# Optimization experiments

Measured on AMD Instinct MI355X. Metric: run time of the kernel, lower is better.

The kernel has to match this reference:

```python
import jax, jax.numpy as jnp
import numpy as np

DIM = 512; VOCAB = 10000; DEPTH = 3
DSTATE = 16; DCONV = 4; EXPAND = 2; HEADS = 8
DINNER = EXPAND * DIM            # 1024
DTRANK = (DIM + 15) // 16        # 32 (mamba_ssm: ceil(d_model/16))
B = 4; L = 1024; CTX = 98
EPS = 1e-5


def layer_norm(x, g, b):
    mu = jnp.mean(x, -1, keepdims=True)
    var = jnp.var(x, -1, keepdims=True)
    return (x - mu) / jnp.sqrt(var + EPS) * g + b


def silu(x):
    return x * jax.nn.sigmoid(x)


def mamba_block(x, in_w, conv_w, conv_b, xproj_w, dt_w, dt_b, A_log, D_skip, out_w):
    # x: [B,L,DIM]
    Bb = x.shape[0]
    xz = x @ in_w.T                              # [B,L,2*DINNER]
    u, z = jnp.split(xz, 2, -1)                  # each [B,L,DINNER]
    # causal depthwise conv1d (pad left d_conv-1)
    uc = jnp.transpose(u, (0, 2, 1))             # [B,DINNER,L]
    uc = jax.lax.conv_general_dilated(
        uc, conv_w, (1,), [(DCONV - 1, 0)],
        dimension_numbers=('NCH', 'OIH', 'NCH'),
        feature_group_count=DINNER)
    u = silu(jnp.transpose(uc, (0, 2, 1)) + conv_b)   # [B,L,DINNER]
    x_dbl = u @ xproj_w.T                        # [B,L,DTRANK+2*DSTATE]
    dt, Bm, Cm = jnp.split(x_dbl, [DTRANK, DTRANK + DSTATE], -1)
    delta = jax.nn.softplus(dt @ dt_w.T + dt_b)  # [B,L,DINNER]
    A = -jnp.exp(A_log)                          # [DINNER,DSTATE]

    def step(h, inp):
        d_t, B_t, C_t, u_t = inp                 # [B,DINNER],[B,DSTATE],[B,DSTATE],[B,DINNER]
        dA = jnp.exp(d_t[..., None] * A)         # [B,DINNER,DSTATE]
        h = dA * h + (d_t * u_t)[..., None] * B_t[:, None, :]
        y_t = jnp.einsum('bds,bs->bd', h, C_t)
        return h, y_t

    h0 = jnp.zeros((Bb, DINNER, DSTATE), x.dtype)
    xs = (jnp.swapaxes(delta, 0, 1), jnp.swapaxes(Bm, 0, 1),
          jnp.swapaxes(Cm, 0, 1), jnp.swapaxes(u, 0, 1))
    _, ys = jax.lax.scan(step, h0, xs)           # ys: [L,B,DINNER]
    y = jnp.swapaxes(ys, 0, 1) + u * D_skip
    y = y * silu(z)
    return y @ out_w.T                           # [B,L,DIM]


def cross_attention(q_in, ctx, in_w, in_b, out_w, out_b):
    Bb, Ln, _ = q_in.shape
    S = ctx.shape[1]
    dh = DIM // HEADS
    wq, wk, wv = jnp.split(in_w, 3, 0)
    bq, bk, bv = jnp.split(in_b, 3, 0)
    q = (q_in @ wq.T + bq).reshape(Bb, Ln, HEADS, dh)
    k = (ctx @ wk.T + bk).reshape(Bb, S, HEADS, dh)
    v = (ctx @ wv.T + bv).reshape(Bb, S, HEADS, dh)
    scale = 1.0 / np.sqrt(dh).astype(np.float32)
    scores = jnp.einsum('blhd,bshd->bhls', q, k) * scale
    attn = jax.nn.softmax(scores, axis=-1)       # [B,H,L,S]
    out = jnp.einsum('bhls,bshd->blhd', attn, v).reshape(Bb, Ln, DIM)
    out = out @ out_w.T + out_b
    return out, attn.mean(axis=1)                # torch MHA averages heads


def setup_inputs() -> dict:
    key = jax.random.key(0)
    ks = jax.random.split(key, 16)
    s = 0.02
    d = {}
    d['x'] = jax.random.randint(ks[0], (B, L), 0, VOCAB)
    d['context'] = jax.random.normal(ks[1], (B, CTX, DIM), jnp.float32)
    d['tok_emb'] = jax.random.normal(ks[2], (VOCAB, DIM), jnp.float32) * s
    d['pos_emb'] = jax.random.normal(ks[3], (1, 1024, DIM), jnp.float32) * s
    d['ln1_g'] = jnp.ones((DEPTH, DIM)); d['ln1_b'] = jnp.zeros((DEPTH, DIM))
    d['in_w'] = jax.random.normal(ks[4], (DEPTH, 2 * DINNER, DIM), jnp.float32) * s
    d['conv_w'] = jax.random.normal(ks[5], (DEPTH, DINNER, 1, DCONV), jnp.float32) * 0.1
    d['conv_b'] = jnp.zeros((DEPTH, DINNER))
    d['xproj_w'] = jax.random.normal(ks[6], (DEPTH, DTRANK + 2 * DSTATE, DINNER), jnp.float32) * s
    d['dt_w'] = jax.random.normal(ks[7], (DEPTH, DINNER, DTRANK), jnp.float32) * 0.1
    d['dt_b'] = jax.random.normal(ks[8], (DEPTH, DINNER), jnp.float32) * 0.1
    # S4D-real init: A_log = log(1..d_state)
    A_log = jnp.log(jnp.arange(1, DSTATE + 1, dtype=jnp.float32))
    d['A_log'] = jnp.broadcast_to(A_log, (DEPTH, DINNER, DSTATE)).copy()
    d['D_skip'] = jnp.ones((DEPTH, DINNER))
    d['mamba_out_w'] = jax.random.normal(ks[9], (DEPTH, DIM, DINNER), jnp.float32) * s
    d['ln2_g'] = jnp.ones((DEPTH, DIM)); d['ln2_b'] = jnp.zeros((DEPTH, DIM))
    d['attn_in_w'] = jax.random.normal(ks[10], (DEPTH, 3 * DIM, DIM), jnp.float32) * s
    d['attn_in_b'] = jnp.zeros((DEPTH, 3 * DIM))
    d['attn_out_w'] = jax.random.normal(ks[11], (DEPTH, DIM, DIM), jnp.float32) * s
    d['attn_out_b'] = jnp.zeros((DEPTH, DIM))
    d['lnf_g'] = jnp.ones((DIM,)); d['lnf_b'] = jnp.zeros((DIM,))
    d['logit_w'] = jax.random.normal(ks[12], (VOCAB, DIM), jnp.float32) * s
    d['logit_b'] = jnp.zeros((VOCAB,))
    return d


def reference(x, context, tok_emb, pos_emb, ln1_g, ln1_b, in_w, conv_w, conv_b,
              xproj_w, dt_w, dt_b, A_log, D_skip, mamba_out_w, ln2_g, ln2_b,
              attn_in_w, attn_in_b, attn_out_w, attn_out_b, lnf_g, lnf_b,
              logit_w, logit_b):
    n = x.shape[1]
    h = tok_emb[x] + pos_emb[:, :n]              # [B,L,DIM]
    all_attn = []
    for i in range(DEPTH):
        h_norm = layer_norm(h, ln1_g[i], ln1_b[i])
        h = h + mamba_block(h_norm, in_w[i], conv_w[i], conv_b[i], xproj_w[i],
                            dt_w[i], dt_b[i], A_log[i], D_skip[i], mamba_out_w[i])
        h_norm = layer_norm(h, ln2_g[i], ln2_b[i])
        attn_out, attn_w = cross_attention(h_norm, context, attn_in_w[i],
                                           attn_in_b[i], attn_out_w[i], attn_out_b[i])
        all_attn.append(attn_w)
        h = h + attn_out
    h = layer_norm(h, lnf_g, lnf_b)
    logits = h @ logit_w.T + logit_b             # [B,L,VOCAB]
    return (logits, tuple(all_attn))
```

## Files before the change

kernel.cpp:

```cpp
#include <hip/hip_runtime.h>
#include <hip/hip_bf16.h>
#include <math.h>

#define DIM 512
#define VOCAB 10000
#define NPAD 10240
#define DEPTH 3
#define DSTATE 16
#define DCONV 4
#define DINNER 1024
#define DTRANK 32
#define BATCH 4
#define SEQ 1024
#define CTX 98
#define HEADS 8
#define DH 64
#define NTOK (BATCH*SEQ)
#define NC 32
#define LC 32
#define KVLD 1024
#define CTXPAD 512

typedef __attribute__((ext_vector_type(8))) short short8;
typedef __attribute__((ext_vector_type(4))) float f32x4;

__device__ __forceinline__ float sigmoidf_(float x){ return 1.f/(1.f+__expf(-x)); }

__device__ __forceinline__ void gload_lds16(const void* g, void* s){
    __builtin_amdgcn_global_load_lds(
        (const __attribute__((address_space(1))) void*)g,
        (__attribute__((address_space(3))) void*)s, 16, 0, 0);
}

__global__ __launch_bounds__(256)
void f2bf_kernel(const float* __restrict__ in, __hip_bfloat16* __restrict__ out)
{
    int i = (blockIdx.x*256 + threadIdx.x)*8;
    float4 a = *(const float4*)(in+i);
    float4 b = *(const float4*)(in+i+4);
    union { __hip_bfloat16 v[8]; short8 s; } o;
    o.v[0]=__float2bfloat16(a.x); o.v[1]=__float2bfloat16(a.y);
    o.v[2]=__float2bfloat16(a.z); o.v[3]=__float2bfloat16(a.w);
    o.v[4]=__float2bfloat16(b.x); o.v[5]=__float2bfloat16(b.y);
    o.v[6]=__float2bfloat16(b.z); o.v[7]=__float2bfloat16(b.w);
    *(short8*)(out+i) = o.s;
}

__global__ __launch_bounds__(128)
void embed_kernel(const int* __restrict__ x,
                  const float* __restrict__ tok_emb,
                  const float* __restrict__ pos_emb,
                  float* __restrict__ h)
{
    int row = blockIdx.x;
    int l = row & (SEQ-1);
    int tok = x[row];
    const float4* te = (const float4*)(tok_emb + (size_t)tok*DIM);
    const float4* pe = (const float4*)(pos_emb + (size_t)l*DIM);
    float4* hp = (float4*)(h + (size_t)row*DIM);
    int i = threadIdx.x;
    float4 a = te[i], b = pe[i];
    hp[i] = make_float4(a.x+b.x, a.y+b.y, a.z+b.z, a.w+b.w);
}

__global__ __launch_bounds__(256)
void layernorm_kernel(const float* __restrict__ in, const float* __restrict__ g,
                      const float* __restrict__ b, __hip_bfloat16* __restrict__ out)
{
    int row = blockIdx.x;
    const float* xr = in + (size_t)row*DIM;
    int t = threadIdx.x;
    float2 v = *(const float2*)(xr + t*2);
    float s  = v.x + v.y;
    float s2 = v.x*v.x + v.y*v.y;
    #pragma unroll
    for (int o=32;o>=1;o>>=1){ s += __shfl_xor(s,o); s2 += __shfl_xor(s2,o); }
    __shared__ float ss[4], ss2[4];
    int w = t>>6;
    if ((t&63)==0){ ss[w]=s; ss2[w]=s2; }
    __syncthreads();
    s  = ss[0]+ss[1]+ss[2]+ss[3];
    s2 = ss2[0]+ss2[1]+ss2[2]+ss2[3];
    float mu  = s * (1.f/DIM);
    float var = s2 * (1.f/DIM) - mu*mu;
    float rstd = rsqrtf(var + 1e-5f);
    float2 gg = *(const float2*)(g + t*2);
    float2 bb = *(const float2*)(b + t*2);
    __hip_bfloat162 o2;
    o2.x = __float2bfloat16((v.x-mu)*rstd*gg.x + bb.x);
    o2.y = __float2bfloat16((v.y-mu)*rstd*gg.y + bb.y);
    *(__hip_bfloat162*)(out + (size_t)row*DIM + t*2) = o2;
}

template<int BIAS, int RES, int NCHECK, int OUTBF>
__global__ __launch_bounds__(256)
void gemm_bf16(const __hip_bfloat16* __restrict__ A, int lda,
               const __hip_bfloat16* __restrict__ W, int ldw,
               const float* __restrict__ bias,
               void* __restrict__ Cv, int ldc, int Nstore, int K)
{
    __shared__ __hip_bfloat16 As[128*32];
    __shared__ __hip_bfloat16 Ws[128*32];
    int t = threadIdx.x;
    int w = t >> 6, l = t & 63;
    int m0 = blockIdx.y*128, n0 = blockIdx.x*128;
    int wm = (w>>1)*64, wn = (w&1)*64;
    int lrow = l & 15, lq = l >> 4;
    f32x4 acc[4][4];
    #pragma unroll
    for (int i=0;i<4;i++)
        #pragma unroll
        for (int j=0;j<4;j++)
            acc[i][j] = (f32x4){0.f,0.f,0.f,0.f};

    for (int k0 = 0; k0 < K; k0 += 32){
        __syncthreads();
        #pragma unroll
        for (int it = 0; it < 2; ++it){
            int p = it*256 + t;
            int r = p >> 2, c = (p & 3)*8;
            gload_lds16(A + (size_t)(m0+r)*lda + k0 + c, As + p*8);
            gload_lds16(W + (size_t)(n0+r)*ldw + k0 + c, Ws + p*8);
        }
        __syncthreads();
        short8 a[4], b[4];
        #pragma unroll
        for (int mt=0;mt<4;mt++)
            a[mt] = *(const short8*)(As + (wm + mt*16 + lrow)*32 + lq*8);
        #pragma unroll
        for (int nt=0;nt<4;nt++)
            b[nt] = *(const short8*)(Ws + (wn + nt*16 + lrow)*32 + lq*8);
        #pragma unroll
        for (int mt=0;mt<4;mt++)
            #pragma unroll
            for (int nt=0;nt<4;nt++)
                acc[mt][nt] = __builtin_amdgcn_mfma_f32_16x16x32_bf16(
                    a[mt], b[nt], acc[mt][nt], 0, 0, 0);
    }
    #pragma unroll
    for (int nt=0;nt<4;nt++){
        int col = n0 + wn + nt*16 + lrow;
        if (NCHECK && col >= Nstore) continue;
        float bv = BIAS ? bias[col] : 0.f;
        #pragma unroll
        for (int mt=0;mt<4;mt++){
            #pragma unroll
            for (int r=0;r<4;r++){
                int row = m0 + wm + mt*16 + lq*4 + r;
                float v = acc[mt][nt][r] + bv;
                if (OUTBF){
                    __hip_bfloat16* cp = (__hip_bfloat16*)Cv + (size_t)row*ldc + col;
                    *cp = __float2bfloat16(v);
                } else {
                    float* cp = (float*)Cv + (size_t)row*ldc + col;
                    if (RES) v += *cp;
                    *cp = v;
                }
            }
        }
    }
}

template<int ACT, int BIAS, int RES>
__global__ __launch_bounds__(256)
void gemm_f32(const float* __restrict__ A, int lda,
              const float* __restrict__ W, int ldw,
              const float* __restrict__ bias,
              float* __restrict__ C, int ldc,
              int M, int N, int K)
{
    __shared__ float As[16][64];
    __shared__ float Ws[16][64];
    int t = threadIdx.x;
    int tx = t & 15, ty = t >> 4;
    int m0 = blockIdx.y * 64, n0 = blockIdx.x * 64;
    int loadRow = t >> 2;
    int loadK   = (t & 3) << 2;
    float acc[4][4] = {};
    for (int k0 = 0; k0 < K; k0 += 16) {
        {
            int gr = m0 + loadRow;
            float4 a4 = make_float4(0.f,0.f,0.f,0.f);
            if (gr < M) a4 = *(const float4*)(A + (size_t)gr*lda + k0 + loadK);
            As[loadK+0][loadRow] = a4.x;
            As[loadK+1][loadRow] = a4.y;
            As[loadK+2][loadRow] = a4.z;
            As[loadK+3][loadRow] = a4.w;
            int gn = n0 + loadRow;
            float4 w4 = make_float4(0.f,0.f,0.f,0.f);
            if (gn < N) w4 = *(const float4*)(W + (size_t)gn*ldw + k0 + loadK);
            Ws[loadK+0][loadRow] = w4.x;
            Ws[loadK+1][loadRow] = w4.y;
            Ws[loadK+2][loadRow] = w4.z;
            Ws[loadK+3][loadRow] = w4.w;
        }
        __syncthreads();
        #pragma unroll
        for (int k = 0; k < 16; ++k) {
            float4 a4 = *(const float4*)&As[k][ty<<2];
            float4 w4 = *(const float4*)&Ws[k][tx<<2];
            float a[4] = {a4.x,a4.y,a4.z,a4.w};
            float w[4] = {w4.x,w4.y,w4.z,w4.w};
            #pragma unroll
            for (int i=0;i<4;i++)
                #pragma unroll
                for (int j=0;j<4;j++)
                    acc[i][j] = fmaf(a[i], w[j], acc[i][j]);
        }
        __syncthreads();
    }
    #pragma unroll
    for (int i=0;i<4;i++){
        int row = m0 + (ty<<2) + i;
        if (row >= M) continue;
        #pragma unroll
        for (int j=0;j<4;j++){
            int col = n0 + (tx<<2) + j;
            if (col >= N) continue;
            float v = acc[i][j];
            if (BIAS) v += bias[col];
            if (ACT==1) v = (v > 20.f) ? v : log1pf(__expf(v));
            float* cp = C + (size_t)row*ldc + col;
            if (RES) v += *cp;
            *cp = v;
        }
    }
}

__global__ __launch_bounds__(256)
void conv_silu_kernel(const float* __restrict__ xz, const float* __restrict__ cw,
                      const float* __restrict__ cb, float* __restrict__ u,
                      __hip_bfloat16* __restrict__ ubf)
{
    int idx = blockIdx.x*256 + threadIdx.x;
    int d = idx & (DINNER-1);
    int row = idx >> 10;
    int l = row & (SEQ-1);
    int bbase = row - l;
    float acc = cb[d];
    #pragma unroll
    for (int k=0;k<DCONV;k++){
        int ls = l - (DCONV-1) + k;
        if (ls >= 0)
            acc = fmaf(xz[((size_t)(bbase+ls))*(2*DINNER) + d], cw[d*DCONV+k], acc);
    }
    float uv = acc * sigmoidf_(acc);
    u[idx] = uv;
    ubf[idx] = __float2bfloat16(uv);
}

__global__ __launch_bounds__(256)
void scan_pass1(const float* __restrict__ delta, const float* __restrict__ u,
                const float* __restrict__ xdbl, const float* __restrict__ A_log,
                float* __restrict__ hend, float* __restrict__ dsum_out)
{
    __shared__ float bc[LC][32];
    int c = blockIdx.x;
    int b = blockIdx.y >> 2, dg = blockIdx.y & 3;
    int t = threadIdx.x;
    int d = dg*256 + t;
    int rowbase = b*SEQ + c*LC;
    for (int idx = t; idx < LC*32; idx += 256){
        int r = idx >> 5, j = idx & 31;
        bc[r][j] = xdbl[(size_t)(rowbase + r)*64 + DTRANK + j];
    }
    float Av[DSTATE];
    #pragma unroll
    for (int s4 = 0; s4 < 4; ++s4){
        float4 a4 = *(const float4*)(A_log + (size_t)d*DSTATE + s4*4);
        Av[s4*4+0] = -__expf(a4.x);
        Av[s4*4+1] = -__expf(a4.y);
        Av[s4*4+2] = -__expf(a4.z);
        Av[s4*4+3] = -__expf(a4.w);
    }
    __syncthreads();
    float h[DSTATE] = {};
    float ds = 0.f;
    for (int tt = 0; tt < LC; ++tt){
        size_t row = (size_t)(rowbase + tt);
        float dlt = delta[row*DINNER + d];
        float uv  = u[row*DINNER + d];
        ds += dlt;
        float du = dlt*uv;
        #pragma unroll
        for (int s = 0; s < DSTATE; ++s)
            h[s] = fmaf(__expf(dlt*Av[s]), h[s], du*bc[tt][s]);
    }
    size_t base = ((size_t)(b*NC + c)*DINNER + d)*DSTATE;
    #pragma unroll
    for (int s4=0;s4<4;s4++)
        *(float4*)(hend + base + s4*4) =
            make_float4(h[s4*4],h[s4*4+1],h[s4*4+2],h[s4*4+3]);
    dsum_out[(size_t)(b*NC+c)*DINNER + d] = ds;
}

__global__ __launch_bounds__(256)
void scan_pass2(const float* __restrict__ hend, const float* __restrict__ dsum,
                const float* __restrict__ A_log, float* __restrict__ hin)
{
    int gid = blockIdx.x*256 + threadIdx.x;
    int s = gid & 15;
    int bd = gid >> 4;
    int d = bd & (DINNER-1);
    int b = bd >> 10;
    float Av = -__expf(A_log[(size_t)d*DSTATE + s]);
    float h = 0.f;
    for (int c = 0; c < NC; ++c){
        size_t idx = ((size_t)(b*NC + c)*DINNER + d)*DSTATE + s;
        hin[idx] = h;
        h = fmaf(__expf(Av*dsum[(size_t)(b*NC+c)*DINNER + d]), h, hend[idx]);
    }
}

__global__ __launch_bounds__(256)
void scan_pass3(const float* __restrict__ delta, const float* __restrict__ u,
                const float* __restrict__ xdbl, const float* __restrict__ xz,
                const float* __restrict__ A_log, const float* __restrict__ D_skip,
                const float* __restrict__ hin, __hip_bfloat16* __restrict__ y)
{
    __shared__ float bc[LC][32];
    int c = blockIdx.x;
    int b = blockIdx.y >> 2, dg = blockIdx.y & 3;
    int t = threadIdx.x;
    int d = dg*256 + t;
    int rowbase = b*SEQ + c*LC;
    for (int idx = t; idx < LC*32; idx += 256){
        int r = idx >> 5, j = idx & 31;
        bc[r][j] = xdbl[(size_t)(rowbase + r)*64 + DTRANK + j];
    }
    float Av[DSTATE];
    #pragma unroll
    for (int s4 = 0; s4 < 4; ++s4){
        float4 a4 = *(const float4*)(A_log + (size_t)d*DSTATE + s4*4);
        Av[s4*4+0] = -__expf(a4.x);
        Av[s4*4+1] = -__expf(a4.y);
        Av[s4*4+2] = -__expf(a4.z);
        Av[s4*4+3] = -__expf(a4.w);
    }
    float h[DSTATE];
    size_t hbase = ((size_t)(b*NC + c)*DINNER + d)*DSTATE;
    #pragma unroll
    for (int s4=0;s4<4;s4++){
        float4 h4 = *(const float4*)(hin + hbase + s4*4);
        h[s4*4+0]=h4.x; h[s4*4+1]=h4.y; h[s4*4+2]=h4.z; h[s4*4+3]=h4.w;
    }
    float Dv = D_skip[d];
    __syncthreads();
    for (int tt = 0; tt < LC; ++tt){
        size_t row = (size_t)(rowbase + tt);
        float dlt = delta[row*DINNER + d];
        float uv  = u[row*DINNER + d];
        float du = dlt*uv;
        float yv = 0.f;
        #pragma unroll
        for (int s = 0; s < DSTATE; ++s){
            h[s] = fmaf(__expf(dlt*Av[s]), h[s], du*bc[tt][s]);
            yv = fmaf(h[s], bc[tt][16+s], yv);
        }
        float zv = xz[row*(2*DINNER) + DINNER + d];
        y[row*DINNER + d] = __float2bfloat16((yv + uv*Dv) * (zv * sigmoidf_(zv)));
    }
}

#define QS_OFF 0
#define KS_OFF 16384
#define VT_OFF 30720
#define PT_OFF 47104
#define SMEM_BYTES 79872

__device__ __forceinline__ int swz(int row, int byteoff){
    return byteoff ^ ((row & 7) << 4);
}

__global__ __launch_bounds__(512)
void attn_mfma_kernel(const __hip_bfloat16* __restrict__ q,
                      const __hip_bfloat16* __restrict__ kv,
                      __hip_bfloat16* __restrict__ outp,
                      float* __restrict__ Pg)
{
    __shared__ alignas(16) char smem[SMEM_BYTES];
    int t = threadIdx.x;
    int bh = blockIdx.x;
    int b = bh >> 3, h = bh & 7;
    int lrow0 = blockIdx.y * 128;
    size_t grow0 = (size_t)b*SEQ + lrow0;

    #pragma unroll
    for (int it = 0; it < 6; ++it)
        *(f32x4*)(smem + VT_OFF + (it*512 + t)*16) = (f32x4){0.f,0.f,0.f,0.f};
    __syncthreads();

    const __hip_bfloat16* qb = q + grow0*DIM + h*DH;
    #pragma unroll
    for (int it = 0; it < 2; ++it){
        int cidx = it*512 + t;
        int row = cidx >> 3, c8 = cidx & 7;
        short8 a = *(const short8*)(qb + (size_t)row*DIM + c8*8);
        *(short8*)(smem + QS_OFF + row*128 + swz(row, c8*16)) = a;
    }
    const __hip_bfloat16* kb = kv + (size_t)(b*CTX)*KVLD + h*DH;
    #pragma unroll
    for (int it = 0; it < 2; ++it){
        int cidx = it*512 + t;
        if (cidx < 112*8){
            int row = cidx >> 3, c8 = cidx & 7;
            short8 a = (short8){0,0,0,0,0,0,0,0};
            if (row < CTX) a = *(const short8*)(kb + (size_t)row*KVLD + c8*8);
            *(short8*)(smem + KS_OFF + row*128 + swz(row, c8*16)) = a;
        }
    }
    const __hip_bfloat16* vb = kv + (size_t)(b*CTX)*KVLD + DIM + h*DH;
    #pragma unroll
    for (int it = 0; it < 4; ++it){
        int c = it*512 + t;
        if (c < 1600){
            int d = c & 63, s4 = c >> 6;
            union { unsigned short hh[4]; unsigned long long u; } pk;
            #pragma unroll
            for (int j = 0; j < 4; ++j){
                int s = s4*4 + j;
                pk.hh[j] = (s < CTX) ? *(const unsigned short*)(vb + (size_t)s*KVLD + d) : 0;
            }
            *(unsigned long long*)(smem + VT_OFF + d*256 + swz(d, s4*8)) = pk.u;
        }
    }
    __syncthreads();

    int w = t >> 6, l = t & 63;
    int lr = l & 15, lq = l >> 4;
    f32x4 acc[7];
    #pragma unroll
    for (int nt = 0; nt < 7; ++nt) acc[nt] = (f32x4){0.f,0.f,0.f,0.f};
    #pragma unroll
    for (int kk = 0; kk < 2; ++kk){
        int arow = w*16 + lr;
        short8 af = *(const short8*)(smem + QS_OFF + arow*128 + swz(arow, kk*64 + lq*16));
        #pragma unroll
        for (int nt = 0; nt < 7; ++nt){
            int brow = nt*16 + lr;
            short8 bf = *(const short8*)(smem + KS_OFF + brow*128 + swz(brow, kk*64 + lq*16));
            acc[nt] = __builtin_amdgcn_mfma_f32_16x16x32_bf16(af, bf, acc[nt], 0, 0, 0);
        }
    }

    float* Pgp = Pg + ((size_t)bh*SEQ + lrow0)*CTX;
    #pragma unroll
    for (int r = 0; r < 4; ++r){
        int row = w*16 + lq*4 + r;
        float vals[7];
        #pragma unroll
        for (int nt = 0; nt < 7; ++nt) vals[nt] = acc[nt][r] * 0.125f;
        if (lr >= 2) vals[6] = -1e30f;
        float m = vals[0];
        #pragma unroll
        for (int nt = 1; nt < 7; ++nt) m = fmaxf(m, vals[nt]);
        #pragma unroll
        for (int o = 8; o >= 1; o >>= 1) m = fmaxf(m, __shfl_xor(m, o));
        float ssum = 0.f;
        #pragma unroll
        for (int nt = 0; nt < 7; ++nt){ vals[nt] = __expf(vals[nt] - m); ssum += vals[nt]; }
        #pragma unroll
        for (int o = 8; o >= 1; o >>= 1) ssum += __shfl_xor(ssum, o);
        float inv = 1.f / ssum;
        #pragma unroll
        for (int nt = 0; nt < 7; ++nt){
            float p = vals[nt] * inv;
            int col = nt*16 + lr;
            *(__hip_bfloat16*)(smem + PT_OFF + row*256 + swz(row, col*2)) = __float2bfloat16(p);
            if (col < CTX) Pgp[(size_t)row*CTX + col] = p;
        }
    }
    __syncthreads();

    f32x4 acc2[4];
    #pragma unroll
    for (int nt = 0; nt < 4; ++nt) acc2[nt] = (f32x4){0.f,0.f,0.f,0.f};
    #pragma unroll
    for (int kk = 0; kk < 4; ++kk){
        int arow = w*16 + lr;
        short8 af = *(const short8*)(smem + PT_OFF + arow*256 + swz(arow, kk*64 + lq*16));
        #pragma unroll
        for (int nt = 0; nt < 4; ++nt){
            int brow = nt*16 + lr;
            short8 bf = *(const short8*)(smem + VT_OFF + brow*256 + swz(brow, kk*64 + lq*16));
            acc2[nt] = __builtin_amdgcn_mfma_f32_16x16x32_bf16(af, bf, acc2[nt], 0, 0, 0);
        }
    }
    #pragma unroll
    for (int nt = 0; nt < 4; ++nt){
        int col = h*DH + nt*16 + lr;
        #pragma unroll
        for (int r = 0; r < 4; ++r){
            int row = w*16 + lq*4 + r;
            outp[(grow0 + row)*DIM + col] = __float2bfloat16(acc2[nt][r]);
        }
    }
}

__global__ __launch_bounds__(256)
void attn_mean_kernel(const float* __restrict__ Pg, float* __restrict__ am)
{
    int idx = blockIdx.x*256 + threadIdx.x;
    int row = idx / CTX;
    int s = idx - row*CTX;
    int b = row >> 10;
    int l = row & (SEQ-1);
    const float* p = Pg + ((size_t)(b*HEADS)*SEQ + l)*CTX + s;
    float acc = 0.f;
    #pragma unroll
    for (int h = 0; h < HEADS; ++h) acc += p[(size_t)h*SEQ*CTX];
    am[idx] = acc * 0.125f;
}

extern "C" void kernel_launch(void* const* d_in, const int* in_sizes, int n_in,
                              void* d_out, int out_size, void* d_ws, size_t ws_size,
                              hipStream_t stream)
{
    (void)in_sizes; (void)n_in; (void)out_size; (void)ws_size;
    const int*   x        = (const int*)  d_in[0];
    const float* context  = (const float*)d_in[1];
    const float* tok_emb  = (const float*)d_in[2];
    const float* pos_emb  = (const float*)d_in[3];
    const float* ln1_g    = (const float*)d_in[4];
    const float* ln1_b    = (const float*)d_in[5];
    const float* in_w     = (const float*)d_in[6];
    const float* conv_w   = (const float*)d_in[7];
    const float* conv_b   = (const float*)d_in[8];
    const float* xproj_w  = (const float*)d_in[9];
    const float* dt_w     = (const float*)d_in[10];
    const float* dt_b     = (const float*)d_in[11];
    const float* A_log    = (const float*)d_in[12];
    const float* D_skip   = (const float*)d_in[13];
    const float* out_w    = (const float*)d_in[14];
    const float* ln2_g    = (const float*)d_in[15];
    const float* ln2_b    = (const float*)d_in[16];
    const float* ain_w    = (const float*)d_in[17];
    const float* ain_b    = (const float*)d_in[18];
    const float* aout_w   = (const float*)d_in[19];
    const float* aout_b   = (const float*)d_in[20];
    const float* lnf_g    = (const float*)d_in[21];
    const float* lnf_b    = (const float*)d_in[22];
    const float* logit_w  = (const float*)d_in[23];
    const float* logit_b  = (const float*)d_in[24];
    float* out = (float*)d_out;

    float* ws = (float*)d_ws;
    size_t off = 0;
    float* hbuf  = ws + off;  off += (size_t)NTOK*DIM;
    float* ubuf  = ws + off;  off += (size_t)NTOK*DINNER;
    float* xdbl  = ws + off;  off += (size_t)NTOK*64;
    float* dbuf  = ws + off;  off += (size_t)NTOK*DINNER;
    __hip_bfloat16* tnorm_bf   = (__hip_bfloat16*)(ws + off); off += (size_t)NTOK*DIM/2;
    __hip_bfloat16* logit_w_bf = (__hip_bfloat16*)(ws + off); off += (size_t)NPAD*DIM/2;
    float* Pgbuf = dbuf;

    float* ob = out;
    float* xz    = ob;                 ob += (size_t)NTOK*2*DINNER;
    float* hend  = ob;                 ob += (size_t)BATCH*NC*DINNER*DSTATE;
    float* hinb  = ob;                 ob += (size_t)BATCH*NC*DINNER*DSTATE;
    float* dsumb = ob;                 ob += (size_t)BATCH*NC*DINNER;
    __hip_bfloat16* bfp = (__hip_bfloat16*)ob;
    __hip_bfloat16* in_w_bf   = bfp;   bfp += (size_t)DEPTH*2*DINNER*DIM;
    __hip_bfloat16* out_w_bf  = bfp;   bfp += (size_t)DEPTH*DIM*DINNER;
    __hip_bfloat16* ainw_bf   = bfp;   bfp += (size_t)DEPTH*3*DIM*DIM;
    __hip_bfloat16* aoutw_bf  = bfp;   bfp += (size_t)DEPTH*DIM*DIM;
    __hip_bfloat16* ybuf_bf   = bfp;   bfp += (size_t)NTOK*DINNER;
    __hip_bfloat16* abuf_bf   = bfp;   bfp += (size_t)NTOK*DIM;
    __hip_bfloat16* qbf       = bfp;   bfp += (size_t)NTOK*DIM;
    __hip_bfloat16* ubf       = bfp;   bfp += (size_t)NTOK*DINNER;
    __hip_bfloat16* ctx_bf    = bfp;   bfp += (size_t)CTXPAD*DIM;
    __hip_bfloat16* kv_bf     = bfp;   bfp += (size_t)CTXPAD*KVLD;
    __hip_bfloat16* xprojw_bf = bfp;   bfp += (size_t)DEPTH*128*DINNER;

    f2bf_kernel<<<(DEPTH*2*DINNER*DIM)/2048, 256, 0, stream>>>(in_w, in_w_bf);
    f2bf_kernel<<<(DEPTH*DIM*DINNER)/2048, 256, 0, stream>>>(out_w, out_w_bf);
    f2bf_kernel<<<(DEPTH*3*DIM*DIM)/2048, 256, 0, stream>>>(ain_w, ainw_bf);
    f2bf_kernel<<<(DEPTH*DIM*DIM)/2048, 256, 0, stream>>>(aout_w, aoutw_bf);
    f2bf_kernel<<<(VOCAB*DIM)/2048, 256, 0, stream>>>(logit_w, logit_w_bf);
    hipMemsetAsync(logit_w_bf + (size_t)VOCAB*DIM, 0,
                   (size_t)(NPAD-VOCAB)*DIM*sizeof(__hip_bfloat16), stream);
    f2bf_kernel<<<(BATCH*CTX*DIM)/2048, 256, 0, stream>>>(context, ctx_bf);
    hipMemsetAsync(ctx_bf + (size_t)BATCH*CTX*DIM, 0,
                   (size_t)(CTXPAD - BATCH*CTX)*DIM*sizeof(__hip_bfloat16), stream);
    hipMemsetAsync(xprojw_bf, 0, (size_t)DEPTH*128*DINNER*sizeof(__hip_bfloat16), stream);
    for (int i = 0; i < DEPTH; ++i)
        f2bf_kernel<<<(64*DINNER)/2048, 256, 0, stream>>>(
            xproj_w + (size_t)i*64*DINNER, xprojw_bf + (size_t)i*128*DINNER);

    embed_kernel<<<NTOK, 128, 0, stream>>>(x, tok_emb, pos_emb, hbuf);

    float* attn_out_base = out + (size_t)NTOK*VOCAB;

    for (int i = 0; i < DEPTH; ++i){
        const float* Ai = A_log + (size_t)i*DINNER*DSTATE;
        layernorm_kernel<<<NTOK, 256, 0, stream>>>(hbuf, ln1_g + i*DIM, ln1_b + i*DIM, tnorm_bf);
        gemm_bf16<0,0,0,0><<<dim3(2*DINNER/128, NTOK/128), 256, 0, stream>>>(
            tnorm_bf, DIM, in_w_bf + (size_t)i*2*DINNER*DIM, DIM, nullptr,
            xz, 2*DINNER, 2*DINNER, DIM);
        conv_silu_kernel<<<(NTOK*DINNER)/256, 256, 0, stream>>>(
            xz, conv_w + (size_t)i*DINNER*DCONV, conv_b + i*DINNER, ubuf, ubf);
        gemm_bf16<0,0,1,0><<<dim3(1, NTOK/128), 256, 0, stream>>>(
            ubf, DINNER, xprojw_bf + (size_t)i*128*DINNER, DINNER, nullptr,
            xdbl, 64, 64, DINNER);
        gemm_f32<1,1,0><<<dim3(DINNER/64, NTOK/64), 256, 0, stream>>>(
            xdbl, 64, dt_w + (size_t)i*DINNER*DTRANK, DTRANK, dt_b + i*DINNER,
            dbuf, DINNER, NTOK, DINNER, DTRANK);
        scan_pass1<<<dim3(NC, BATCH*4), 256, 0, stream>>>(
            dbuf, ubuf, xdbl, Ai, hend, dsumb);
        scan_pass2<<<(BATCH*DINNER*DSTATE)/256, 256, 0, stream>>>(
            hend, dsumb, Ai, hinb);
        scan_pass3<<<dim3(NC, BATCH*4), 256, 0, stream>>>(
            dbuf, ubuf, xdbl, xz, Ai, D_skip + i*DINNER, hinb, ybuf_bf);
        gemm_bf16<0,1,0,0><<<dim3(DIM/128, NTOK/128), 256, 0, stream>>>(
            ybuf_bf, DINNER, out_w_bf + (size_t)i*DIM*DINNER, DINNER, nullptr,
            hbuf, DIM, DIM, DINNER);
        layernorm_kernel<<<NTOK, 256, 0, stream>>>(hbuf, ln2_g + i*DIM, ln2_b + i*DIM, tnorm_bf);
        gemm_bf16<1,0,0,1><<<dim3(DIM/128, NTOK/128), 256, 0, stream>>>(
            tnorm_bf, DIM, ainw_bf + (size_t)i*3*DIM*DIM, DIM, ain_b + (size_t)i*3*DIM,
            qbf, DIM, DIM, DIM);
        gemm_bf16<1,0,0,1><<<dim3(KVLD/128, CTXPAD/128), 256, 0, stream>>>(
            ctx_bf, DIM, ainw_bf + (size_t)i*3*DIM*DIM + (size_t)DIM*DIM, DIM,
            ain_b + (size_t)i*3*DIM + DIM, kv_bf, KVLD, KVLD, DIM);
        attn_mfma_kernel<<<dim3(BATCH*HEADS, SEQ/128), 512, 0, stream>>>(
            qbf, kv_bf, abuf_bf, Pgbuf);
        attn_mean_kernel<<<(NTOK*CTX)/256, 256, 0, stream>>>(
            Pgbuf, attn_out_base + (size_t)i*NTOK*CTX);
        gemm_bf16<1,1,0,0><<<dim3(DIM/128, NTOK/128), 256, 0, stream>>>(
            abuf_bf, DIM, aoutw_bf + (size_t)i*DIM*DIM, DIM, aout_b + i*DIM,
            hbuf, DIM, DIM, DIM);
    }
    layernorm_kernel<<<NTOK, 256, 0, stream>>>(hbuf, lnf_g, lnf_b, tnorm_bf);
    gemm_bf16<1,0,1,0><<<dim3(NPAD/128, NTOK/128), 256, 0, stream>>>(
        tnorm_bf, DIM, logit_w_bf, DIM, logit_b, out, VOCAB, VOCAB, DIM);
}
```

Baseline: 1.131 ms.

## Merge weight conversions, batch KV projections across layers, split-K the x_proj GEMM

All fp32-to-bf16 weight and context conversions and the zero-padding memsets are merged into one prep kernel. The three per-layer K/V projections of the fixed context become a single batched GEMM launch, using a new z-dimension offset scheme in gemm_bf16. The narrow x_proj GEMM, which previously ran only 32 blocks, is split four ways along K into partial buffers and summed by a small reduce kernel. This is meant to cut launch count and raise parallelism, at the cost of extra partial-sum traffic and a larger kv buffer.

```diff
diff --git a/kernel.cpp b/kernel.cpp
--- a/kernel.cpp
+++ b/kernel.cpp
@@ -20,6 +20,7 @@
 #define LC 32
 #define KVLD 1024
 #define CTXPAD 512
+#define XKS 4
 
 typedef __attribute__((ext_vector_type(8))) short short8;
 typedef __attribute__((ext_vector_type(4))) float f32x4;
@@ -32,18 +33,66 @@
         (__attribute__((address_space(3))) void*)s, 16, 0, 0);
 }
 
-__global__ __launch_bounds__(256)
-void f2bf_kernel(const float* __restrict__ in, __hip_bfloat16* __restrict__ out)
-{
-    int i = (blockIdx.x*256 + threadIdx.x)*8;
-    float4 a = *(const float4*)(in+i);
-    float4 b = *(const float4*)(in+i+4);
-    union { __hip_bfloat16 v[8]; short8 s; } o;
+__device__ __forceinline__ void cvt8(const float* __restrict__ s, __hip_bfloat16* __restrict__ d){
+    float4 a = *(const float4*)s;
+    float4 b = *(const float4*)(s+4);
+    union { __hip_bfloat16 v[8]; short8 x; } o;
     o.v[0]=__float2bfloat16(a.x); o.v[1]=__float2bfloat16(a.y);
     o.v[2]=__float2bfloat16(a.z); o.v[3]=__float2bfloat16(a.w);
     o.v[4]=__float2bfloat16(b.x); o.v[5]=__float2bfloat16(b.y);
     o.v[6]=__float2bfloat16(b.z); o.v[7]=__float2bfloat16(b.w);
-    *(short8*)(out+i) = o.s;
+    *(short8*)d = o.x;
+}
+__device__ __forceinline__ void zero8(__hip_bfloat16* __restrict__ d){
+    *(short8*)d = (short8){0,0,0,0,0,0,0,0};
+}
+
+#define N_INW   (DEPTH*2*DINNER*DIM)
+#define N_OUTW  (DEPTH*DIM*DINNER)
+#define N_AINW  (DEPTH*3*DIM*DIM)
+#define N_AOUTW (DEPTH*DIM*DIM)
+#define N_LOGIT (NPAD*DIM)
+#define N_CTX   (CTXPAD*DIM)
+#define N_XPROJ (DEPTH*128*DINNER)
+#define N_PREP_TOTAL (N_INW+N_OUTW+N_AINW+N_AOUTW+N_LOGIT+N_CTX+N_XPROJ)
+
+__global__ __launch_bounds__(256)
+void prep_kernel(const float* __restrict__ in_w,   __hip_bfloat16* __restrict__ in_w_bf,
+                 const float* __restrict__ out_w,  __hip_bfloat16* __restrict__ out_w_bf,
+                 const float* __restrict__ ain_w,  __hip_bfloat16* __restrict__ ainw_bf,
+                 const float* __restrict__ aout_w, __hip_bfloat16* __restrict__ aoutw_bf,
+                 const float* __restrict__ logit_w,__hip_bfloat16* __restrict__ logit_w_bf,
+                 const float* __restrict__ context,__hip_bfloat16* __restrict__ ctx_bf,
+                 const float* __restrict__ xproj_w,__hip_bfloat16* __restrict__ xprojw_bf)
+{
+    int i = (blockIdx.x*256 + threadIdx.x)*8;
+    if (i < N_INW){ cvt8(in_w + i, in_w_bf + i); return; }
+    i -= N_INW;
+    if (i < N_OUTW){ cvt8(out_w + i, out_w_bf + i); return; }
+    i -= N_OUTW;
+    if (i < N_AINW){ cvt8(ain_w + i, ainw_bf + i); return; }
+    i -= N_AINW;
+    if (i < N_AOUTW){ cvt8(aout_w + i, aoutw_bf + i); return; }
+    i -= N_AOUTW;
+    if (i < N_LOGIT){
+        if (i < VOCAB*DIM) cvt8(logit_w + i, logit_w_bf + i);
+        else zero8(logit_w_bf + i);
+        return;
+    }
+    i -= N_LOGIT;
+    if (i < N_CTX){
+        if (i < BATCH*CTX*DIM) cvt8(context + i, ctx_bf + i);
+        else zero8(ctx_bf + i);
+        return;
+    }
+    i -= N_CTX;
+    {
+        int layer = i >> 17;
+        int rem   = i & 131071;
+        int inrow = rem >> 10;
+        if (inrow < 64) cvt8(xproj_w + (layer<<16) + rem, xprojw_bf + i);
+        else            zero8(xprojw_bf + i);
+    }
 }
 
 __global__ __launch_bounds__(128)
@@ -97,11 +146,16 @@
 void gemm_bf16(const __hip_bfloat16* __restrict__ A, int lda,
                const __hip_bfloat16* __restrict__ W, int ldw,
                const float* __restrict__ bias,
-               void* __restrict__ Cv, int ldc, int Nstore, int K)
+               void* __restrict__ Cv, int ldc, int Nstore, int K,
+               size_t az, size_t wz, size_t cz, size_t bz)
 {
     __shared__ __hip_bfloat16 As[128*32];
     __shared__ __hip_bfloat16 Ws[128*32];
     int t = threadIdx.x;
+    int z = blockIdx.z;
+    const __hip_bfloat16* Ap = A + (size_t)z*az;
+    const __hip_bfloat16* Wp = W + (size_t)z*wz;
+    size_t coff = (size_t)z*cz;
     int w = t >> 6, l = t & 63;
     int m0 = blockIdx.y*128, n0 = blockIdx.x*128;
     int wm = (w>>1)*64, wn = (w&1)*64;
@@ -119,8 +173,8 @@
         for (int it = 0; it < 2; ++it){
             int p = it*256 + t;
             int r = p >> 2, c = (p & 3)*8;
-            gload_lds16(A + (size_t)(m0+r)*lda + k0 + c, As + p*8);
-            gload_lds16(W + (size_t)(n0+r)*ldw + k0 + c, Ws + p*8);
+            gload_lds16(Ap + (size_t)(m0+r)*lda + k0 + c, As + p*8);
+            gload_lds16(Wp + (size_t)(n0+r)*ldw + k0 + c, Ws + p*8);
         }
         __syncthreads();
         short8 a[4], b[4];
@@ -141,7 +195,7 @@
     for (int nt=0;nt<4;nt++){
         int col = n0 + wn + nt*16 + lrow;
         if (NCHECK && col >= Nstore) continue;
-        float bv = BIAS ? bias[col] : 0.f;
+        float bv = BIAS ? bias[(size_t)z*bz + col] : 0.f;
         #pragma unroll
         for (int mt=0;mt<4;mt++){
             #pragma unroll
@@ -149,16 +203,29 @@
                 int row = m0 + wm + mt*16 + lq*4 + r;
                 float v = acc[mt][nt][r] + bv;
                 if (OUTBF){
-                    __hip_bfloat16* cp = (__hip_bfloat16*)Cv + (size_t)row*ldc + col;
+                    __hip_bfloat16* cp = (__hip_bfloat16*)Cv + coff + (size_t)row*ldc + col;
                     *cp = __float2bfloat16(v);
                 } else {
-                    float* cp = (float*)Cv + (size_t)row*ldc + col;
+                    float* cp = (float*)Cv + coff + (size_t)row*ldc + col;
                     if (RES) v += *cp;
                     *cp = v;
                 }
             }
         }
     }
+}
+
+__global__ __launch_bounds__(256)
+void xreduce_kernel(const float* __restrict__ p, float* __restrict__ o)
+{
+    int i = (blockIdx.x*256 + threadIdx.x)*4;
+    const size_t S = (size_t)NTOK*64;
+    float4 a = *(const float4*)(p+i);
+    float4 b = *(const float4*)(p+i+S);
+    float4 c = *(const float4*)(p+i+2*S);
+    float4 d = *(const float4*)(p+i+3*S);
+    *(float4*)(o+i) = make_float4(a.x+b.x+c.x+d.x, a.y+b.y+c.y+d.y,
+                                  a.z+b.z+c.z+d.z, a.w+b.w+c.w+d.w);
 }
 
 template<int ACT, int BIAS, int RES>
@@ -550,6 +617,7 @@
     float* ubuf  = ws + off;  off += (size_t)NTOK*DINNER;
     float* xdbl  = ws + off;  off += (size_t)NTOK*64;
     float* dbuf  = ws + off;  off += (size_t)NTOK*DINNER;
+    float* xpart = ws + off;  off += (size_t)XKS*NTOK*64;
     __hip_bfloat16* tnorm_bf   = (__hip_bfloat16*)(ws + off); off += (size_t)NTOK*DIM/2;
     __hip_bfloat16* logit_w_bf = (__hip_bfloat16*)(ws + off); off += (size_t)NPAD*DIM/2;
     float* Pgbuf = dbuf;
@@ -560,34 +628,28 @@
     float* hinb  = ob;                 ob += (size_t)BATCH*NC*DINNER*DSTATE;
     float* dsumb = ob;                 ob += (size_t)BATCH*NC*DINNER;
     __hip_bfloat16* bfp = (__hip_bfloat16*)ob;
-    __hip_bfloat16* in_w_bf   = bfp;   bfp += (size_t)DEPTH*2*DINNER*DIM;
-    __hip_bfloat16* out_w_bf  = bfp;   bfp += (size_t)DEPTH*DIM*DINNER;
-    __hip_bfloat16* ainw_bf   = bfp;   bfp += (size_t)DEPTH*3*DIM*DIM;
-    __hip_bfloat16* aoutw_bf  = bfp;   bfp += (size_t)DEPTH*DIM*DIM;
+    __hip_bfloat16* in_w_bf   = bfp;   bfp += (size_t)N_INW;
+    __hip_bfloat16* out_w_bf  = bfp;   bfp += (size_t)N_OUTW;
+    __hip_bfloat16* ainw_bf   = bfp;   bfp += (size_t)N_AINW;
+    __hip_bfloat16* aoutw_bf  = bfp;   bfp += (size_t)N_AOUTW;
     __hip_bfloat16* ybuf_bf   = bfp;   bfp += (size_t)NTOK*DINNER;
     __hip_bfloat16* abuf_bf   = bfp;   bfp += (size_t)NTOK*DIM;
     __hip_bfloat16* qbf       = bfp;   bfp += (size_t)NTOK*DIM;
     __hip_bfloat16* ubf       = bfp;   bfp += (size_t)NTOK*DINNER;
-    __hip_bfloat16* ctx_bf    = bfp;   bfp += (size_t)CTXPAD*DIM;
-    __hip_bfloat16* kv_bf     = bfp;   bfp += (size_t)CTXPAD*KVLD;
-    __hip_bfloat16* xprojw_bf = bfp;   bfp += (size_t)DEPTH*128*DINNER;
-
-    f2bf_kernel<<<(DEPTH*2*DINNER*DIM)/2048, 256, 0, stream>>>(in_w, in_w_bf);
-    f2bf_kernel<<<(DEPTH*DIM*DINNER)/2048, 256, 0, stream>>>(out_w, out_w_bf);
-    f2bf_kernel<<<(DEPTH*3*DIM*DIM)/2048, 256, 0, stream>>>(ain_w, ainw_bf);
-    f2bf_kernel<<<(DEPTH*DIM*DIM)/2048, 256, 0, stream>>>(aout_w, aoutw_bf);
-    f2bf_kernel<<<(VOCAB*DIM)/2048, 256, 0, stream>>>(logit_w, logit_w_bf);
-    hipMemsetAsync(logit_w_bf + (size_t)VOCAB*DIM, 0,
-                   (size_t)(NPAD-VOCAB)*DIM*sizeof(__hip_bfloat16), stream);
-    f2bf_kernel<<<(BATCH*CTX*DIM)/2048, 256, 0, stream>>>(context, ctx_bf);
-    hipMemsetAsync(ctx_bf + (size_t)BATCH*CTX*DIM, 0,
-                   (size_t)(CTXPAD - BATCH*CTX)*DIM*sizeof(__hip_bfloat16), stream);
-    hipMemsetAsync(xprojw_bf, 0, (size_t)DEPTH*128*DINNER*sizeof(__hip_bfloat16), stream);
-    for (int i = 0; i < DEPTH; ++i)
-        f2bf_kernel<<<(64*DINNER)/2048, 256, 0, stream>>>(
-            xproj_w + (size_t)i*64*DINNER, xprojw_bf + (size_t)i*128*DINNER);
+    __hip_bfloat16* ctx_bf    = bfp;   bfp += (size_t)N_CTX;
+    __hip_bfloat16* kv_bf     = bfp;   bfp += (size_t)DEPTH*CTXPAD*KVLD;
+    __hip_bfloat16* xprojw_bf = bfp;   bfp += (size_t)N_XPROJ;
+
+    prep_kernel<<<N_PREP_TOTAL/2048, 256, 0, stream>>>(
+        in_w, in_w_bf, out_w, out_w_bf, ain_w, ainw_bf, aout_w, aoutw_bf,
+        logit_w, logit_w_bf, context, ctx_bf, xproj_w, xprojw_bf);
 
     embed_kernel<<<NTOK, 128, 0, stream>>>(x, tok_emb, pos_emb, hbuf);
+
+    gemm_bf16<1,0,0,1><<<dim3(KVLD/128, CTXPAD/128, DEPTH), 256, 0, stream>>>(
+        ctx_bf, DIM, ainw_bf + (size_t)DIM*DIM, DIM, ain_b + DIM,
+        kv_bf, KVLD, KVLD, DIM,
+        0, (size_t)3*DIM*DIM, (size_t)CTXPAD*KVLD, (size_t)3*DIM);
 
     float* attn_out_base = out + (size_t)NTOK*VOCAB;
 
@@ -596,12 +658,14 @@
         layernorm_kernel<<<NTOK, 256, 0, stream>>>(hbuf, ln1_g + i*DIM, ln1_b + i*DIM, tnorm_bf);
         gemm_bf16<0,0,0,0><<<dim3(2*DINNER/128, NTOK/128), 256, 0, stream>>>(
             tnorm_bf, DIM, in_w_bf + (size_t)i*2*DINNER*DIM, DIM, nullptr,
-            xz, 2*DINNER, 2*DINNER, DIM);
+            xz, 2*DINNER, 2*DINNER, DIM, 0, 0, 0, 0);
         conv_silu_kernel<<<(NTOK*DINNER)/256, 256, 0, stream>>>(
             xz, conv_w + (size_t)i*DINNER*DCONV, conv_b + i*DINNER, ubuf, ubf);
-        gemm_bf16<0,0,1,0><<<dim3(1, NTOK/128), 256, 0, stream>>>(
+        gemm_bf16<0,0,1,0><<<dim3(1, NTOK/128, XKS), 256, 0, stream>>>(
             ubf, DINNER, xprojw_bf + (size_t)i*128*DINNER, DINNER, nullptr,
-            xdbl, 64, 64, DINNER);
+            xpart, 64, 64, DINNER/XKS,
+            (size_t)(DINNER/XKS), (size_t)(DINNER/XKS), (size_t)NTOK*64, 0);
+        xreduce_kernel<<<(NTOK*64)/1024, 256, 0, stream>>>(xpart, xdbl);
         gemm_f32<1,1,0><<<dim3(DINNER/64, NTOK/64), 256, 0, stream>>>(
             xdbl, 64, dt_w + (size_t)i*DINNER*DTRANK, DTRANK, dt_b + i*DINNER,
             dbuf, DINNER, NTOK, DINNER, DTRANK);
@@ -613,23 +677,20 @@
             dbuf, ubuf, xdbl, xz, Ai, D_skip + i*DINNER, hinb, ybuf_bf);
         gemm_bf16<0,1,0,0><<<dim3(DIM/128, NTOK/128), 256, 0, stream>>>(
             ybuf_bf, DINNER, out_w_bf + (size_t)i*DIM*DINNER, DINNER, nullptr,
-            hbuf, DIM, DIM, DINNER);
+            hbuf, DIM, DIM, DINNER, 0, 0, 0, 0);
         layernorm_kernel<<<NTOK, 256, 0, stream>>>(hbuf, ln2_g + i*DIM, ln2_b + i*DIM, tnorm_bf);
         gemm_bf16<1,0,0,1><<<dim3(DIM/128, NTOK/128), 256, 0, stream>>>(
             tnorm_bf, DIM, ainw_bf + (size_t)i*3*DIM*DIM, DIM, ain_b + (size_t)i*3*DIM,
-            qbf, DIM, DIM, DIM);
-        gemm_bf16<1,0,0,1><<<dim3(KVLD/128, CTXPAD/128), 256, 0, stream>>>(
-            ctx_bf, DIM, ainw_bf + (size_t)i*3*DIM*DIM + (size_t)DIM*DIM, DIM,
-            ain_b + (size_t)i*3*DIM + DIM, kv_bf, KVLD, KVLD, DIM);
+            qbf, DIM, DIM, DIM, 0, 0, 0, 0);
         attn_mfma_kernel<<<dim3(BATCH*HEADS, SEQ/128), 512, 0, stream>>>(
-            qbf, kv_bf, abuf_bf, Pgbuf);
+            qbf, kv_bf + (size_t)i*CTXPAD*KVLD, abuf_bf, Pgbuf);
         attn_mean_kernel<<<(NTOK*CTX)/256, 256, 0, stream>>>(
             Pgbuf, attn_out_base + (size_t)i*NTOK*CTX);
         gemm_bf16<1,1,0,0><<<dim3(DIM/128, NTOK/128), 256, 0, stream>>>(
             abuf_bf, DIM, aoutw_bf + (size_t)i*DIM*DIM, DIM, aout_b + i*DIM,
-            hbuf, DIM, DIM, DIM);
+            hbuf, DIM, DIM, DIM, 0, 0, 0, 0);
     }
     layernorm_kernel<<<NTOK, 256, 0, stream>>>(hbuf, lnf_g, lnf_b, tnorm_bf);
     gemm_bf16<1,0,1,0><<<dim3(NPAD/128, NTOK/128), 256, 0, stream>>>(
-        tnorm_bf, DIM, logit_w_bf, DIM, logit_b, out, VOCAB, VOCAB, DIM);
-}
+        tnorm_bf, DIM, logit_w_bf, DIM, logit_b, out, VOCAB, VOCAB, DIM, 0, 0, 0, 0);
+}
```

Measured after the change: 1.051 ms. 1.08x faster.
